# Kernel optimization log

Measured on AMD Instinct MI355X. Metric: run time of the kernel, lower is better.

The kernel has to match this reference:

```python
import jax, jax.numpy as jnp
import numpy as np

B, S, D = 4, 4096, 1024
EXPAND = 2
D_INNER = EXPAND * D          # 2048
D_CONV = 4
CHUNK = 64
H = 16
DH = D // H                   # 64
EPS = 1e-5


def setup_inputs() -> dict:
    key = jax.random.key(0)
    ks = jax.random.split(key, 10)
    s = 0.02
    return {
        "x": jax.random.normal(ks[0], (B, S, D), jnp.float32),
        "norm_w": jnp.ones((D,), jnp.float32),
        "w_up": jax.random.normal(ks[1], (D, D_INNER), jnp.float32) * s,
        "w_gate": jax.random.normal(ks[2], (D, D_INNER), jnp.float32) * s,
        "w_down": jax.random.normal(ks[3], (D_INNER, D), jnp.float32) * s,
        "conv_w": jax.random.normal(ks[4], (D_INNER, 1, D_CONV), jnp.float32) * s,
        "conv_b": jnp.zeros((D_INNER,), jnp.float32),
        "wq": jax.random.normal(ks[5], (D, D), jnp.float32) * s,
        "wk": jax.random.normal(ks[6], (D, D), jnp.float32) * s,
        "wv": jax.random.normal(ks[7], (D, D), jnp.float32) * s,
        "wo": jax.random.normal(ks[8], (D, D), jnp.float32) * s,
    }


def rmsnorm(x, w):
    var = jnp.mean(jnp.square(x.astype(jnp.float32)), axis=-1, keepdims=True)
    return (x * jax.lax.rsqrt(var + EPS).astype(x.dtype)) * w


def causal_dwconv(x, w, b):
    # x: [B, S, C] -> depthwise causal conv along S
    y = jax.lax.conv_general_dilated(
        x.transpose(0, 2, 1), w,
        window_strides=(1,), padding=[(D_CONV - 1, 0)],
        feature_group_count=D_INNER,
        dimension_numbers=("NCH", "OIH", "NCH"))
    return (y + b[None, :, None]).transpose(0, 2, 1)


def hebbian_memory(h, wq, wk, wv, wo):
    # chunked Hebbian associative memory: M += phi(k)^T v, read y = phi(q) M (+ intra-chunk causal)
    phi = lambda t: jax.nn.elu(t) + 1.0
    q = phi((h @ wq).reshape(B, S, H, DH)) * (DH ** -0.5)
    k = phi((h @ wk).reshape(B, S, H, DH))
    v = (h @ wv).reshape(B, S, H, DH)

    def to_chunks(t):  # [B,S,H,DH] -> [N, B, H, CHUNK, DH]
        return t.reshape(B, S // CHUNK, CHUNK, H, DH).transpose(1, 0, 3, 2, 4)

    qc, kc, vc = to_chunks(q), to_chunks(k), to_chunks(v)
    mask = jnp.tril(jnp.ones((CHUNK, CHUNK), bool))

    def step(M, inp):
        qb, kb, vb = inp                                   # [B,H,C,DH]
        inter = jnp.einsum("bhcd,bhde->bhce", qb, M)       # read from past memory
        sc = jnp.einsum("bhcd,bhed->bhce", qb, kb)
        sc = jnp.where(mask, sc, 0.0)                      # causal intra-chunk Hebbian read
        intra = jnp.einsum("bhce,bhed->bhcd", sc, vb)
        M = M + jnp.einsum("bhcd,bhce->bhde", kb, vb)      # Hebbian outer-product write
        return M, inter + intra

    M0 = jnp.zeros((B, H, DH, DH), h.dtype)
    _, y = jax.lax.scan(step, M0, (qc, kc, vc))            # y: [N,B,H,C,DH]
    y = y.transpose(1, 0, 3, 2, 4).reshape(B, S, D)
    return y @ wo


def reference(x, norm_w, w_up, w_gate, w_down, conv_w, conv_b, wq, wk, wv, wo):
    normed = rmsnorm(x, norm_w)
    val = jax.nn.silu(causal_dwconv(normed @ w_up, conv_w, conv_b))   # conv local mixing
    h = (jax.nn.silu(normed @ w_gate) * val) @ w_down                 # gated MLP
    out = hebbian_memory(h, wq, wk, wv, wo)                           # associative memory
    return x + out
```

## Files before the change

kernel.cpp:

```cpp
#include <hip/hip_runtime.h>
#include <hip/hip_fp16.h>
#include <cstdint>

#define NRALL 16384
#define DM    1024
#define DI    2048
#define SEQL  4096

typedef _Float16 f16;
typedef _Float16 f16x8 __attribute__((ext_vector_type(8)));
typedef _Float16 f16x4 __attribute__((ext_vector_type(4)));
typedef float    f32x4 __attribute__((ext_vector_type(4)));

__device__ __forceinline__ float phi_f(float t)  { return t > 0.0f ? t + 1.0f : __expf(t); }
__device__ __forceinline__ float silu_f(float t) { return t / (1.0f + __expf(-t)); }

#define GLDS16(g, l)                                                            \
    __builtin_amdgcn_global_load_lds(                                           \
        (const __attribute__((address_space(1))) void*)(g),                     \
        (__attribute__((address_space(3))) void*)(l), 16, 0, 0)

#define FMA4(dst, s, vv)                      \
    dst.x = fmaf((s), (vv).x, dst.x);         \
    dst.y = fmaf((s), (vv).y, dst.y);         \
    dst.z = fmaf((s), (vv).z, dst.z);         \
    dst.w = fmaf((s), (vv).w, dst.w);

__global__ __launch_bounds__(256) void rmsnorm_k(const float* __restrict__ x,
                                                 const float* __restrict__ nw,
                                                 f16* __restrict__ xn)
{
    const int r = blockIdx.x, t = threadIdx.x;
    const float4 v = *(const float4*)(x + (size_t)r * DM + t * 4);
    float s = v.x * v.x + v.y * v.y + v.z * v.z + v.w * v.w;
#pragma unroll
    for (int m = 1; m < 64; m <<= 1) s += __shfl_xor(s, m);
    __shared__ float ws4[4];
    if ((t & 63) == 0) ws4[t >> 6] = s;
    __syncthreads();
    const float tot = ws4[0] + ws4[1] + ws4[2] + ws4[3];
    const float sc = rsqrtf(tot * (1.0f / DM) + 1e-5f);
    const float4 w = *(const float4*)(nw + t * 4);
    f16x4 o;
    o[0] = (f16)(v.x * sc * w.x); o[1] = (f16)(v.y * sc * w.y);
    o[2] = (f16)(v.z * sc * w.z); o[3] = (f16)(v.w * sc * w.w);
    *(f16x4*)(xn + (size_t)r * DM + t * 4) = o;
}

__device__ __forceinline__ void wfmt_one(const float* __restrict__ W, char* __restrict__ fmt,
                                         int n, int kt, int Nw, int Ntot, int noff)
{
    const int ng = noff + n;
#pragma unroll
    for (int kh = 0; kh < 2; ++kh) {
        char* o = fmt + ((size_t)(kt * 2 + kh) * Ntot + ng) * 64;
#pragma unroll
        for (int c2 = 0; c2 < 4; ++c2) {
            f16x8 p;
#pragma unroll
            for (int j = 0; j < 8; ++j)
                p[j] = (f16)W[(size_t)(kt * 64 + kh * 32 + c2 * 8 + j) * Nw + n];
            *(f16x8*)(o + ((c2 ^ ((ng >> 1) & 3)) << 4)) = p;
        }
    }
}

__global__ __launch_bounds__(256) void wfmt_all_k(const float* __restrict__ w_up,
                                                  const float* __restrict__ w_gate,
                                                  const float* __restrict__ w_down,
                                                  const float* __restrict__ wq,
                                                  const float* __restrict__ wk,
                                                  const float* __restrict__ wv,
                                                  const float* __restrict__ wo,
                                                  char* __restrict__ fmtUG,
                                                  char* __restrict__ fmtD,
                                                  char* __restrict__ fmtQKV,
                                                  char* __restrict__ fmtO)
{
    int id = blockIdx.x;
    const int t = threadIdx.x;
    if (id < 128) { wfmt_one(w_up,   fmtUG,  (id % 8) * 256 + t, id / 8, DI, 4096, 0);    return; }
    id -= 128;
    if (id < 128) { wfmt_one(w_gate, fmtUG,  (id % 8) * 256 + t, id / 8, DI, 4096, 2048); return; }
    id -= 128;
    if (id < 128) { wfmt_one(w_down, fmtD,   (id % 4) * 256 + t, id / 4, DM, 1024, 0);    return; }
    id -= 128;
    if (id < 64)  { wfmt_one(wq,     fmtQKV, (id % 4) * 256 + t, id / 4, DM, 3072, 0);    return; }
    id -= 64;
    if (id < 64)  { wfmt_one(wk,     fmtQKV, (id % 4) * 256 + t, id / 4, DM, 3072, 1024); return; }
    id -= 64;
    if (id < 64)  { wfmt_one(wv,     fmtQKV, (id % 4) * 256 + t, id / 4, DM, 3072, 2048); return; }
    id -= 64;
    wfmt_one(wo, fmtO, (id % 4) * 256 + t, id / 4, DM, 1024, 0);
}

#define PHASE(p, ks, mh, STAGE_STMT, VM)                                          \
    {                                                                             \
        if ((mh) == 0) {                                                          \
            _Pragma("unroll")                                                     \
            for (int q = 0; q < 4; ++q) {                                         \
                const int row = wm * 128 + q * 16 + lr16;                         \
                af[q] = *(const f16x8*)(ldsb + (p) * 32768 + (ks) * 16384         \
                          + row * 64 + ((kb ^ ((row >> 1) & 3)) << 4));           \
                const int n = wn * 64 + q * 16 + lr16;                            \
                bf[q] = *(const f16x8*)(ldsb + 65536 + (p) * 32768 + (ks) * 16384 \
                          + n * 64 + ((kb ^ ((n >> 1) & 3)) << 4));               \
            }                                                                     \
        } else {                                                                  \
            _Pragma("unroll")                                                     \
            for (int q = 0; q < 4; ++q) {                                         \
                const int row = wm * 128 + (q + 4) * 16 + lr16;                   \
                af[q] = *(const f16x8*)(ldsb + (p) * 32768 + (ks) * 16384         \
                          + row * 64 + ((kb ^ ((row >> 1) & 3)) << 4));           \
            }                                                                     \
        }                                                                         \
        STAGE_STMT;                                                               \
        if (VM) asm volatile("s_waitcnt vmcnt(4)" ::: "memory");                  \
        __builtin_amdgcn_sched_barrier(0);                                        \
        __builtin_amdgcn_s_barrier();                                             \
        asm volatile("s_waitcnt lgkmcnt(0)" ::: "memory");                        \
        __builtin_amdgcn_sched_barrier(0);                                        \
        __builtin_amdgcn_s_setprio(1);                                            \
        _Pragma("unroll")                                                         \
        for (int q = 0; q < 4; ++q) {                                             \
            acc[(mh) * 4 + q][0] = __builtin_amdgcn_mfma_f32_16x16x32_f16(        \
                af[q], bf[0], acc[(mh) * 4 + q][0], 0, 0, 0);                     \
            acc[(mh) * 4 + q][1] = __builtin_amdgcn_mfma_f32_16x16x32_f16(        \
                af[q], bf[1], acc[(mh) * 4 + q][1], 0, 0, 0);                     \
            acc[(mh) * 4 + q][2] = __builtin_amdgcn_mfma_f32_16x16x32_f16(        \
                af[q], bf[2], acc[(mh) * 4 + q][2], 0, 0, 0);                     \
            acc[(mh) * 4 + q][3] = __builtin_amdgcn_mfma_f32_16x16x32_f16(        \
                af[q], bf[3], acc[(mh) * 4 + q][3], 0, 0, 0);                     \
        }                                                                         \
        __builtin_amdgcn_s_setprio(0);                                            \
        __builtin_amdgcn_sched_barrier(0);                                        \
    }

template <int EPI>
__global__ __launch_bounds__(512, 2) void mg256_k(const f16* __restrict__ A, int lda,
                                                  const char* __restrict__ fmt,
                                                  void* __restrict__ Cv,
                                                  int N, int K, int gx,
                                                  const float* __restrict__ addx)
{
    __shared__ __align__(16) char ldsb[131072];

    const int t = threadIdx.x;
    int wid = blockIdx.x;
    { const int cpx = gridDim.x >> 3; wid = (wid & 7) * cpx + (wid >> 3); }
    const int bx = wid % gx, by = wid / gx;
    const int bm = by * 256, bn = bx * 256;
    const int lane = t & 63, wv = t >> 6;
    const int wm = wv >> 2, wn = wv & 3;
    const int kb = lane >> 4, lr16 = lane & 15;
    const int NT = K >> 6;

    f32x4 acc[8][4];
#pragma unroll
    for (int i = 0; i < 8; ++i)
#pragma unroll
        for (int j = 0; j < 4; ++j) acc[i][j] = (f32x4)0.0f;

    auto STAGE_A = [&](int p, int kh, int kt) {
#pragma unroll
        for (int r = 0; r < 2; ++r) {
            const int idx = (r * 8 + wv) * 64;
            const int ii = idx + lane;
            const int row = ii >> 2, sl = ii & 3;
            const int c2 = sl ^ ((row >> 1) & 3);
            const f16* src = A + (size_t)(bm + row) * lda + kt * 64 + kh * 32 + c2 * 8;
            GLDS16(src, ldsb + p * 32768 + kh * 16384 + idx * 16);
        }
    };
    auto STAGE_B = [&](int p, int kh, int kt) {
#pragma unroll
        for (int r = 0; r < 2; ++r) {
            const int idx = (r * 8 + wv) * 64;
            const char* src = fmt + ((size_t)(kt * 2 + kh) * N + bn) * 64 + (size_t)(idx + lane) * 16;
            GLDS16(src, ldsb + 65536 + p * 32768 + kh * 16384 + idx * 16);
        }
    };

    STAGE_A(0, 0, 0); STAGE_B(0, 0, 0);
    STAGE_A(0, 1, 0); STAGE_B(0, 1, 0);
    const int t1p = NT > 1 ? 1 : 0;
    STAGE_A(1, 0, t1p); STAGE_B(1, 0, t1p);
    asm volatile("s_waitcnt vmcnt(4)" ::: "memory");
    __builtin_amdgcn_s_barrier();
    __builtin_amdgcn_sched_barrier(0);

    f16x8 af[4], bf[4];
    const int NI = NT >> 1;
    for (int i = 0; i < NI; ++i) {
        const int t1 = 2 * i + 1;
        const int t2 = 2 * i + 2 < NT ? 2 * i + 2 : NT - 1;
        const int t3 = 2 * i + 3 < NT ? 2 * i + 3 : NT - 1;
        PHASE(0, 0, 0, STAGE_B(1, 1, t1), 0)
        PHASE(0, 0, 1, STAGE_A(1, 1, t1), 0)
        PHASE(0, 1, 0, STAGE_B(0, 0, t2), 0)
        PHASE(0, 1, 1, STAGE_A(0, 0, t2), 1)
        PHASE(1, 0, 0, STAGE_B(0, 1, t2), 0)
        PHASE(1, 0, 1, STAGE_A(0, 1, t2), 0)
        PHASE(1, 1, 0, STAGE_B(1, 0, t3), 0)
        PHASE(1, 1, 1, STAGE_A(1, 0, t3), 1)
    }
    asm volatile("s_waitcnt vmcnt(0)" ::: "memory");

#pragma unroll
    for (int fm = 0; fm < 8; ++fm) {
        const int row0 = bm + wm * 128 + fm * 16 + kb * 4;
#pragma unroll
        for (int fn = 0; fn < 4; ++fn) {
            const int col = bn + wn * 64 + fn * 16 + lr16;
#pragma unroll
            for (int r = 0; r < 4; ++r) {
                float o = acc[fm][fn][r];
                if (EPI == 1) {
                    if (col < DM) o = phi_f(o) * 0.125f;
                    else if (col < 2 * DM) o = phi_f(o);
                }
                if (EPI == 2) {
                    ((float*)Cv)[(size_t)(row0 + r) * N + col] =
                        o + addx[(size_t)(row0 + r) * N + col];
                } else {
                    ((f16*)Cv)[(size_t)(row0 + r) * N + col] = (f16)o;
                }
            }
        }
    }
}

__global__ __launch_bounds__(256) void conv_gate_k(f16* __restrict__ upg,
                                                   const float* __restrict__ cw,
                                                   const float* __restrict__ cb)
{
    const int r0 = blockIdx.x * 16;
    const int c = threadIdx.x * 8;
    float bias[8];
    {
        const float4 b0 = *(const float4*)(cb + c);
        const float4 b1 = *(const float4*)(cb + c + 4);
        bias[0] = b0.x; bias[1] = b0.y; bias[2] = b0.z; bias[3] = b0.w;
        bias[4] = b1.x; bias[5] = b1.y; bias[6] = b1.z; bias[7] = b1.w;
    }
    float tap[8][4];
#pragma unroll
    for (int j = 0; j < 8; ++j)
        *(float4*)tap[j] = *(const float4*)(cw + (size_t)(c + j) * 4);

    const bool lead = (r0 & (SEQL - 1)) == 0;
    f16x8 w0, w1, w2;
    if (lead) {
        w0 = (f16x8)(f16)0; w1 = (f16x8)(f16)0; w2 = (f16x8)(f16)0;
    } else {
        w0 = *(const f16x8*)(upg + (size_t)(r0 - 3) * 4096 + c);
        w1 = *(const f16x8*)(upg + (size_t)(r0 - 2) * 4096 + c);
        w2 = *(const f16x8*)(upg + (size_t)(r0 - 1) * 4096 + c);
    }
#pragma unroll 4
    for (int i = 0; i < 16; ++i) {
        const size_t row = (size_t)(r0 + i);
        const f16x8 w3 = *(const f16x8*)(upg + row * 4096 + c);
        const f16x8 g  = *(const f16x8*)(upg + row * 4096 + 2048 + c);
        f16x8 o;
#pragma unroll
        for (int j = 0; j < 8; ++j) {
            float a = bias[j];
            a = fmaf((float)w0[j], tap[j][0], a);
            a = fmaf((float)w1[j], tap[j][1], a);
            a = fmaf((float)w2[j], tap[j][2], a);
            a = fmaf((float)w3[j], tap[j][3], a);
            o[j] = (f16)(silu_f((float)g[j]) * silu_f(a));
        }
        *(f16x8*)(upg + row * 4096 + 2048 + c) = o;
        w0 = w1; w1 = w2; w2 = w3;
    }
}

__global__ __launch_bounds__(256) void gscan_g_k(const f16* __restrict__ qkv,
                                                 float* __restrict__ G)
{
    __shared__ float Ks[4096];
    __shared__ float Vs[4096];
    const int t = threadIdx.x, ch = blockIdx.x, h = blockIdx.y, b = blockIdx.z;
    const int r = t >> 2, c16 = (t & 3) * 16;
    const f16* kp = qkv + ((size_t)b * SEQL + ch * 64 + r) * 3072 + DM + h * 64 + c16;
#pragma unroll
    for (int i = 0; i < 2; ++i) {
        const f16x8 kv = *(const f16x8*)(kp + 8 * i);
        const f16x8 vv = *(const f16x8*)(kp + DM + 8 * i);
#pragma unroll
        for (int j = 0; j < 8; ++j) {
            Ks[r * 64 + c16 + 8 * i + j] = (float)kv[j];
            Vs[r * 64 + c16 + 8 * i + j] = (float)vv[j];
        }
    }
    __syncthreads();
    const int d4 = (t >> 4) * 4, e4 = (t & 15) * 4;
    float4 ag[4] = {};
#pragma unroll 4
    for (int c = 0; c < 64; ++c) {
        float ka[4];
        *(float4*)ka = *(const float4*)(Ks + c * 64 + d4);
        const float4 va = *(const float4*)(Vs + c * 64 + e4);
        FMA4(ag[0], ka[0], va);
        FMA4(ag[1], ka[1], va);
        FMA4(ag[2], ka[2], va);
        FMA4(ag[3], ka[3], va);
    }
    float* go = G + (((size_t)b * 16 + h) * 64 + ch) * 4096 + d4 * 64 + e4;
#pragma unroll
    for (int i = 0; i < 4; ++i) *(float4*)(go + i * 64) = ag[i];
}

__global__ __launch_bounds__(256) void gprefix_k(float* __restrict__ G)
{
    const int bh = blockIdx.x >> 4, sl = blockIdx.x & 15;
    const int idx = sl * 256 + threadIdx.x;
    float run = 0.0f;
    float* p = G + (size_t)bh * 64 * 4096 + idx;
#pragma unroll 4
    for (int ch = 0; ch < 64; ++ch) {
        const float g = *p;
        *p = run;
        run += g;
        p += 4096;
    }
}

__global__ __launch_bounds__(256) void gscan_y_k(const f16* __restrict__ qkv,
                                                 const float* __restrict__ G,
                                                 f16* __restrict__ y)
{
    __shared__ float qT[4096];
    __shared__ float Kd[4096];
    __shared__ float Vs[4096];
    __shared__ float Ms[4096];
    const int t = threadIdx.x, ch = blockIdx.x, h = blockIdx.y, b = blockIdx.z;
    const int r = t >> 2, c16 = (t & 3) * 16;
    const f16* qp = qkv + ((size_t)b * SEQL + ch * 64 + r) * 3072 + h * 64 + c16;
#pragma unroll
    for (int i = 0; i < 2; ++i) {
        const f16x8 qv = *(const f16x8*)(qp + 8 * i);
        const f16x8 kv = *(const f16x8*)(qp + DM + 8 * i);
        const f16x8 vv = *(const f16x8*)(qp + 2 * DM + 8 * i);
#pragma unroll
        for (int j = 0; j < 8; ++j) {
            qT[(c16 + 8 * i + j) * 64 + r] = (float)qv[j];
            Kd[(c16 + 8 * i + j) * 64 + r] = (float)kv[j];
            Vs[r * 64 + c16 + 8 * i + j] = (float)vv[j];
        }
    }
    const float* mg = G + (((size_t)b * 16 + h) * 64 + ch) * 4096;
#pragma unroll
    for (int i = 0; i < 4; ++i)
        *(float4*)(Ms + t * 16 + 4 * i) = *(const float4*)(mg + t * 16 + 4 * i);
    __syncthreads();

    const int c4 = (t >> 4) * 4, e4 = (t & 15) * 4;
    float sa[4][4] = {}, ya[4][4] = {};
#pragma unroll 2
    for (int d = 0; d < 64; ++d) {
        float a[4], bb[4], m[4];
        *(float4*)a = *(const float4*)(qT + d * 64 + c4);
        *(float4*)bb = *(const float4*)(Kd + d * 64 + e4);
        *(float4*)m = *(const float4*)(Ms + d * 64 + e4);
#pragma unroll
        for (int i = 0; i < 4; ++i)
#pragma unroll
            for (int j = 0; j < 4; ++j) {
                sa[i][j] = fmaf(a[i], bb[j], sa[i][j]);
                ya[i][j] = fmaf(a[i], m[j], ya[i][j]);
            }
    }
#pragma unroll
    for (int i = 0; i < 4; ++i)
#pragma unroll
        for (int j = 0; j < 4; ++j)
            if (e4 + j > c4 + i) sa[i][j] = 0.0f;
    __syncthreads();
#pragma unroll
    for (int i = 0; i < 4; ++i)
#pragma unroll
        for (int j = 0; j < 4; ++j)
            qT[(e4 + j) * 64 + c4 + i] = sa[i][j];
    __syncthreads();
#pragma unroll 2
    for (int e = 0; e < 64; ++e) {
        float a[4], vv[4];
        *(float4*)a = *(const float4*)(qT + e * 64 + c4);
        *(float4*)vv = *(const float4*)(Vs + e * 64 + e4);
#pragma unroll
        for (int i = 0; i < 4; ++i)
#pragma unroll
            for (int j = 0; j < 4; ++j)
                ya[i][j] = fmaf(a[i], vv[j], ya[i][j]);
    }
#pragma unroll
    for (int i = 0; i < 4; ++i) {
        f16x4 o;
        o[0] = (f16)ya[i][0]; o[1] = (f16)ya[i][1];
        o[2] = (f16)ya[i][2]; o[3] = (f16)ya[i][3];
        *(f16x4*)(y + ((size_t)b * SEQL + ch * 64 + c4 + i) * DM + h * 64 + e4) = o;
    }
}

extern "C" void kernel_launch(void* const* d_in, const int* in_sizes, int n_in,
                              void* d_out, int out_size, void* d_ws, size_t ws_size,
                              hipStream_t stream)
{
    const float* x      = (const float*)d_in[0];
    const float* norm_w = (const float*)d_in[1];
    const float* w_up   = (const float*)d_in[2];
    const float* w_gate = (const float*)d_in[3];
    const float* w_down = (const float*)d_in[4];
    const float* conv_w = (const float*)d_in[5];
    const float* conv_b = (const float*)d_in[6];
    const float* wq     = (const float*)d_in[7];
    const float* wk     = (const float*)d_in[8];
    const float* wv     = (const float*)d_in[9];
    const float* wo     = (const float*)d_in[10];
    float* out = (float*)d_out;

    const size_t BIG_NEED = 247463936ull;
    const bool big = ws_size >= BIG_NEED;

    if (big) {
        char* p = (char*)d_ws;
        f16* upg = (f16*)p;               p += (size_t)NRALL * 4096 * 2;
        f16* hb  = (f16*)p;               p += (size_t)NRALL * DM * 2;
        char* fmtD   = p;                 p += (size_t)64 * 1024 * 64;
        char* fmtQKV = p;                 p += (size_t)32 * 3072 * 64;
        char* fmtO   = p;                 p += (size_t)32 * 1024 * 64;
        f16* xn = (f16*)p;                p += (size_t)NRALL * DM * 2;
        char* fmtUG  = p;
        float* G = (float*)xn;
        f16* qkvb = upg;
        f16* yb   = hb;

        rmsnorm_k<<<NRALL, 256, 0, stream>>>(x, norm_w, xn);
        wfmt_all_k<<<640, 256, 0, stream>>>(w_up, w_gate, w_down, wq, wk, wv, wo,
                                            fmtUG, fmtD, fmtQKV, fmtO);

        mg256_k<0><<<16 * 64, 512, 0, stream>>>(xn, DM, fmtUG, upg, 4096, DM, 16, nullptr);
        conv_gate_k<<<NRALL / 16, 256, 0, stream>>>(upg, conv_w, conv_b);
        mg256_k<0><<<4 * 64, 512, 0, stream>>>(upg + 2048, 4096, fmtD, hb, 1024, DI, 4, nullptr);
        mg256_k<1><<<12 * 64, 512, 0, stream>>>(hb, DM, fmtQKV, qkvb, 3072, DM, 12, nullptr);

        gscan_g_k<<<dim3(64, 16, 4), 256, 0, stream>>>(qkvb, G);
        gprefix_k<<<1024, 256, 0, stream>>>(G);
        gscan_y_k<<<dim3(64, 16, 4), 256, 0, stream>>>(qkvb, G, yb);

        mg256_k<2><<<4 * 64, 512, 0, stream>>>(yb, DM, fmtO, out, 1024, DM, 4, x);
    } else {
        char* p = (char*)d_ws;
        f16* xn = (f16*)p;                p += (size_t)NRALL * DM * 2;
        f16* upg = (f16*)p;               p += (size_t)SEQL * 4096 * 2;
        f16* hb  = (f16*)p;               p += (size_t)SEQL * DM * 2;
        float* G = (float*)p;             p += (size_t)16 * 64 * 4096 * 4;
        char* fmtUG  = p;                 p += (size_t)32 * 4096 * 64;
        char* fmtD   = p;                 p += (size_t)64 * 1024 * 64;
        char* fmtQKV = p;                 p += (size_t)32 * 3072 * 64;
        char* fmtO   = p;
        f16* qkvb = upg;
        f16* yb   = hb;

        rmsnorm_k<<<NRALL, 256, 0, stream>>>(x, norm_w, xn);
        wfmt_all_k<<<640, 256, 0, stream>>>(w_up, w_gate, w_down, wq, wk, wv, wo,
                                            fmtUG, fmtD, fmtQKV, fmtO);

        for (int b = 0; b < 4; ++b) {
            const f16* xnb = xn + (size_t)b * SEQL * DM;
            mg256_k<0><<<16 * 16, 512, 0, stream>>>(xnb, DM, fmtUG, upg, 4096, DM, 16, nullptr);
            conv_gate_k<<<SEQL / 16, 256, 0, stream>>>(upg, conv_w, conv_b);
            mg256_k<0><<<4 * 16, 512, 0, stream>>>(upg + 2048, 4096, fmtD, hb, 1024, DI, 4, nullptr);
            mg256_k<1><<<12 * 16, 512, 0, stream>>>(hb, DM, fmtQKV, qkvb, 3072, DM, 12, nullptr);
            gscan_g_k<<<dim3(64, 16, 1), 256, 0, stream>>>(qkvb, G);
            gprefix_k<<<256, 256, 0, stream>>>(G);
            gscan_y_k<<<dim3(64, 16, 1), 256, 0, stream>>>(qkvb, G, yb);
            mg256_k<2><<<4 * 16, 512, 0, stream>>>(yb, DM, fmtO,
                                                   out + (size_t)b * SEQL * DM, 1024, DM, 4,
                                                   x + (size_t)b * SEQL * DM);
        }
    }
}
```

Baseline: 613.3 us.

## Double-buffer LDS fragment prefetch in GEMM and store chunk memory states as fp16

The GEMM main loop now keeps two register sets of A and B fragments. Each phase prefetches the next phase's fragments from LDS while the current MFMAs run, and the block barrier moves to the end of the phase. This is meant to hide LDS read latency behind matrix math, at the cost of more VGPRs and a more fragile waitcnt/barrier ordering. Separately, the per-chunk Hebbian memory buffer G is stored in fp16 instead of fp32, halving its traffic in the scan, prefix and read kernels but adding rounding error to the accumulated memory prefix.

```diff
diff --git a/kernel.cpp b/kernel.cpp
--- a/kernel.cpp
+++ b/kernel.cpp
@@ -94,46 +94,47 @@
     wfmt_one(wo, fmtO, (id % 4) * 256 + t, id / 4, DM, 1024, 0);
 }
 
-#define PHASE(p, ks, mh, STAGE_STMT, VM)                                          \
+#define PREF_A(aset_, p, ks, rbase)                                               \
+    _Pragma("unroll")                                                             \
+    for (int q = 0; q < 4; ++q) {                                                 \
+        const int row = wm * 128 + ((rbase) + q) * 16 + lr16;                     \
+        afr[aset_][q] = *(const f16x8*)(ldsb + (p) * 32768 + (ks) * 16384         \
+                        + row * 64 + ((kb ^ ((row >> 1) & 3)) << 4));             \
+    }
+#define PREF_B(bset_, p, ks)                                                      \
+    _Pragma("unroll")                                                             \
+    for (int q = 0; q < 4; ++q) {                                                 \
+        const int n = wn * 64 + q * 16 + lr16;                                    \
+        bfr[bset_][q] = *(const f16x8*)(ldsb + 65536 + (p) * 32768 + (ks) * 16384 \
+                        + n * 64 + ((kb ^ ((n >> 1) & 3)) << 4));                 \
+    }
+
+#define PHASE(mh, AS, BS, PREF_STMT, STAGE_STMT, VM)                              \
     {                                                                             \
-        if ((mh) == 0) {                                                          \
-            _Pragma("unroll")                                                     \
-            for (int q = 0; q < 4; ++q) {                                         \
-                const int row = wm * 128 + q * 16 + lr16;                         \
-                af[q] = *(const f16x8*)(ldsb + (p) * 32768 + (ks) * 16384         \
-                          + row * 64 + ((kb ^ ((row >> 1) & 3)) << 4));           \
-                const int n = wn * 64 + q * 16 + lr16;                            \
-                bf[q] = *(const f16x8*)(ldsb + 65536 + (p) * 32768 + (ks) * 16384 \
-                          + n * 64 + ((kb ^ ((n >> 1) & 3)) << 4));               \
-            }                                                                     \
-        } else {                                                                  \
-            _Pragma("unroll")                                                     \
-            for (int q = 0; q < 4; ++q) {                                         \
-                const int row = wm * 128 + (q + 4) * 16 + lr16;                   \
-                af[q] = *(const f16x8*)(ldsb + (p) * 32768 + (ks) * 16384         \
-                          + row * 64 + ((kb ^ ((row >> 1) & 3)) << 4));           \
-            }                                                                     \
+        asm volatile("s_waitcnt lgkmcnt(0)" ::: "memory");                        \
+        __builtin_amdgcn_sched_barrier(0);                                        \
+        if (VM) {                                                                 \
+            asm volatile("s_waitcnt vmcnt(4)" ::: "memory");                      \
+            __builtin_amdgcn_sched_barrier(0);                                    \
         }                                                                         \
+        PREF_STMT;                                                                \
         STAGE_STMT;                                                               \
-        if (VM) asm volatile("s_waitcnt vmcnt(4)" ::: "memory");                  \
-        __builtin_amdgcn_sched_barrier(0);                                        \
-        __builtin_amdgcn_s_barrier();                                             \
-        asm volatile("s_waitcnt lgkmcnt(0)" ::: "memory");                        \
         __builtin_amdgcn_sched_barrier(0);                                        \
         __builtin_amdgcn_s_setprio(1);                                            \
         _Pragma("unroll")                                                         \
         for (int q = 0; q < 4; ++q) {                                             \
             acc[(mh) * 4 + q][0] = __builtin_amdgcn_mfma_f32_16x16x32_f16(        \
-                af[q], bf[0], acc[(mh) * 4 + q][0], 0, 0, 0);                     \
+                afr[AS][q], bfr[BS][0], acc[(mh) * 4 + q][0], 0, 0, 0);           \
             acc[(mh) * 4 + q][1] = __builtin_amdgcn_mfma_f32_16x16x32_f16(        \
-                af[q], bf[1], acc[(mh) * 4 + q][1], 0, 0, 0);                     \
+                afr[AS][q], bfr[BS][1], acc[(mh) * 4 + q][1], 0, 0, 0);           \
             acc[(mh) * 4 + q][2] = __builtin_amdgcn_mfma_f32_16x16x32_f16(        \
-                af[q], bf[2], acc[(mh) * 4 + q][2], 0, 0, 0);                     \
+                afr[AS][q], bfr[BS][2], acc[(mh) * 4 + q][2], 0, 0, 0);           \
             acc[(mh) * 4 + q][3] = __builtin_amdgcn_mfma_f32_16x16x32_f16(        \
-                af[q], bf[3], acc[(mh) * 4 + q][3], 0, 0, 0);                     \
+                afr[AS][q], bfr[BS][3], acc[(mh) * 4 + q][3], 0, 0, 0);           \
         }                                                                         \
         __builtin_amdgcn_s_setprio(0);                                            \
         __builtin_amdgcn_sched_barrier(0);                                        \
+        __builtin_amdgcn_s_barrier();                                             \
     }
 
 template <int EPI>
@@ -181,28 +182,30 @@
         }
     };
 
-    STAGE_A(0, 0, 0); STAGE_B(0, 0, 0);
-    STAGE_A(0, 1, 0); STAGE_B(0, 1, 0);
-    const int t1p = NT > 1 ? 1 : 0;
-    STAGE_A(1, 0, t1p); STAGE_B(1, 0, t1p);
-    asm volatile("s_waitcnt vmcnt(4)" ::: "memory");
+    f16x8 afr[2][4], bfr[2][4];
+
+    const int T1 = NT > 1 ? 1 : 0;
+    STAGE_B(0, 0, 0); STAGE_A(0, 0, 0); STAGE_B(0, 1, 0); STAGE_A(0, 1, 0);
+    STAGE_B(1, 0, T1); STAGE_A(1, 0, T1); STAGE_B(1, 1, T1);
+    asm volatile("s_waitcnt vmcnt(10)" ::: "memory");
     __builtin_amdgcn_s_barrier();
     __builtin_amdgcn_sched_barrier(0);
-
-    f16x8 af[4], bf[4];
+    PREF_A(0, 0, 0, 0);
+    PREF_B(0, 0, 0);
+
     const int NI = NT >> 1;
     for (int i = 0; i < NI; ++i) {
-        const int t1 = 2 * i + 1;
-        const int t2 = 2 * i + 2 < NT ? 2 * i + 2 : NT - 1;
-        const int t3 = 2 * i + 3 < NT ? 2 * i + 3 : NT - 1;
-        PHASE(0, 0, 0, STAGE_B(1, 1, t1), 0)
-        PHASE(0, 0, 1, STAGE_A(1, 1, t1), 0)
-        PHASE(0, 1, 0, STAGE_B(0, 0, t2), 0)
-        PHASE(0, 1, 1, STAGE_A(0, 0, t2), 1)
-        PHASE(1, 0, 0, STAGE_B(0, 1, t2), 0)
-        PHASE(1, 0, 1, STAGE_A(0, 1, t2), 0)
-        PHASE(1, 1, 0, STAGE_B(1, 0, t3), 0)
-        PHASE(1, 1, 1, STAGE_A(1, 0, t3), 1)
+        const int tc = 2 * i + 1;
+        const int ta = 2 * i + 2 < NT ? 2 * i + 2 : NT - 1;
+        const int tb = 2 * i + 3 < NT ? 2 * i + 3 : NT - 1;
+        PHASE(0, 0, 0, PREF_A(1, 0, 0, 4),                    STAGE_A(1, 1, tc), 0)
+        PHASE(1, 1, 0, PREF_A(0, 0, 1, 0); PREF_B(1, 0, 1),   STAGE_B(0, 0, ta), 1)
+        PHASE(0, 0, 1, PREF_A(1, 0, 1, 4),                    STAGE_A(0, 0, ta), 0)
+        PHASE(1, 1, 1, PREF_A(0, 1, 0, 0); PREF_B(0, 1, 0),   STAGE_B(0, 1, ta), 1)
+        PHASE(0, 0, 0, PREF_A(1, 1, 0, 4),                    STAGE_A(0, 1, ta), 0)
+        PHASE(1, 1, 0, PREF_A(0, 1, 1, 0); PREF_B(1, 1, 1),   STAGE_B(1, 0, tb), 1)
+        PHASE(0, 0, 1, PREF_A(1, 1, 1, 4),                    STAGE_A(1, 0, tb), 0)
+        PHASE(1, 1, 1, PREF_A(0, 0, 0, 0); PREF_B(0, 0, 0),   STAGE_B(1, 1, tb), 1)
     }
     asm volatile("s_waitcnt vmcnt(0)" ::: "memory");
 
@@ -278,7 +281,7 @@
 }
 
 __global__ __launch_bounds__(256) void gscan_g_k(const f16* __restrict__ qkv,
-                                                 float* __restrict__ G)
+                                                 f16* __restrict__ G)
 {
     __shared__ float Ks[4096];
     __shared__ float Vs[4096];
@@ -308,28 +311,33 @@
         FMA4(ag[2], ka[2], va);
         FMA4(ag[3], ka[3], va);
     }
-    float* go = G + (((size_t)b * 16 + h) * 64 + ch) * 4096 + d4 * 64 + e4;
-#pragma unroll
-    for (int i = 0; i < 4; ++i) *(float4*)(go + i * 64) = ag[i];
-}
-
-__global__ __launch_bounds__(256) void gprefix_k(float* __restrict__ G)
+    f16* go = G + (((size_t)b * 16 + h) * 64 + ch) * 4096 + d4 * 64 + e4;
+#pragma unroll
+    for (int i = 0; i < 4; ++i) {
+        f16x4 o;
+        o[0] = (f16)ag[i].x; o[1] = (f16)ag[i].y;
+        o[2] = (f16)ag[i].z; o[3] = (f16)ag[i].w;
+        *(f16x4*)(go + i * 64) = o;
+    }
+}
+
+__global__ __launch_bounds__(256) void gprefix_k(f16* __restrict__ G)
 {
     const int bh = blockIdx.x >> 4, sl = blockIdx.x & 15;
     const int idx = sl * 256 + threadIdx.x;
     float run = 0.0f;
-    float* p = G + (size_t)bh * 64 * 4096 + idx;
+    f16* p = G + (size_t)bh * 64 * 4096 + idx;
 #pragma unroll 4
     for (int ch = 0; ch < 64; ++ch) {
-        const float g = *p;
-        *p = run;
+        const float g = (float)*p;
+        *p = (f16)run;
         run += g;
         p += 4096;
     }
 }
 
 __global__ __launch_bounds__(256) void gscan_y_k(const f16* __restrict__ qkv,
-                                                 const float* __restrict__ G,
+                                                 const f16* __restrict__ G,
                                                  f16* __restrict__ y)
 {
     __shared__ float qT[4096];
@@ -351,10 +359,13 @@
             Vs[r * 64 + c16 + 8 * i + j] = (float)vv[j];
         }
     }
-    const float* mg = G + (((size_t)b * 16 + h) * 64 + ch) * 4096;
-#pragma unroll
-    for (int i = 0; i < 4; ++i)
-        *(float4*)(Ms + t * 16 + 4 * i) = *(const float4*)(mg + t * 16 + 4 * i);
+    const f16* mg = G + (((size_t)b * 16 + h) * 64 + ch) * 4096;
+#pragma unroll
+    for (int i = 0; i < 2; ++i) {
+        const f16x8 mv = *(const f16x8*)(mg + t * 16 + 8 * i);
+#pragma unroll
+        for (int j = 0; j < 8; ++j) Ms[t * 16 + 8 * i + j] = (float)mv[j];
+    }
     __syncthreads();
 
     const int c4 = (t >> 4) * 4, e4 = (t & 15) * 4;
@@ -434,7 +445,7 @@
         char* fmtO   = p;                 p += (size_t)32 * 1024 * 64;
         f16* xn = (f16*)p;                p += (size_t)NRALL * DM * 2;
         char* fmtUG  = p;
-        float* G = (float*)xn;
+        f16* G = (f16*)xn;
         f16* qkvb = upg;
         f16* yb   = hb;
 
@@ -457,7 +468,7 @@
         f16* xn = (f16*)p;                p += (size_t)NRALL * DM * 2;
         f16* upg = (f16*)p;               p += (size_t)SEQL * 4096 * 2;
         f16* hb  = (f16*)p;               p += (size_t)SEQL * DM * 2;
-        float* G = (float*)p;             p += (size_t)16 * 64 * 4096 * 4;
+        f16* G = (f16*)p;                 p += (size_t)16 * 64 * 4096 * 2;
         char* fmtUG  = p;                 p += (size_t)32 * 4096 * 64;
         char* fmtD   = p;                 p += (size_t)64 * 1024 * 64;
         char* fmtQKV = p;                 p += (size_t)32 * 3072 * 64;
```

After: 612.9 us. Within noise of the previous version (-0.1%).
